# Kernel optimization log

Measured on AMD Instinct MI355X. Metric: run time of the kernel, lower is better.

## Reference

```python
import jax, jax.numpy as jnp
import numpy as np

B, H, W, C, F = 8, 128, 128, 256, 256

def setup_inputs() -> dict:
    key = jax.random.key(0)
    k1, k2, k3 = jax.random.split(key, 3)
    x = jax.random.normal(k1, (B, H, W, C), dtype=jnp.float32)
    style = jax.random.normal(k2, (B, 1, 1, C), dtype=jnp.float32)
    # he_uniform over fan_in = 3*3*C
    limit = np.sqrt(6.0 / (3 * 3 * C)).astype(np.float32)
    kernel = jax.random.uniform(k3, (3, 3, C, F), dtype=jnp.float32, minval=-limit, maxval=limit)
    return {"x": x, "style": style, "kernel": kernel}

def reference(x, style, kernel):
    b, h, w_, c = x.shape
    f = kernel.shape[-1]
    # per-sample modulation: [B,1,1,C,1] * [1,3,3,C,F] -> [B,3,3,C,F]
    wmod = kernel[None] * (style[..., None] + 1.0)
    demod = jnp.sqrt(jnp.sum(jnp.square(wmod), axis=(1, 2, 3), keepdims=True) + 1e-8)
    wmod = wmod / demod
    # grouped conv trick: x -> [1, B*C, H, W], filters -> [3,3,C,B*F], groups=B
    xg = jnp.transpose(x, (0, 3, 1, 2)).reshape(1, b * c, h, w_)
    wf = jnp.transpose(wmod, (1, 2, 3, 0, 4)).reshape(3, 3, c, b * f)
    y = jax.lax.conv_general_dilated(
        xg, wf, window_strides=(1, 1), padding='SAME',
        dimension_numbers=('NCHW', 'HWIO', 'NCHW'),
        feature_group_count=b)
    y = y.reshape(b, f, h, w_)
    return jnp.transpose(y, (0, 2, 3, 1))
```

## Files before the change

kernel.cpp:

```cpp
#include <hip/hip_runtime.h>
#include <hip/hip_bf16.h>


#define NB 8
#define NH 128
#define NW 128
#define NC 256
#define NF 256

typedef __attribute__((ext_vector_type(8))) short bf16x8;
typedef __attribute__((ext_vector_type(4))) float f32x4;

#define PA 2080
#define A_ROW (4 * PA)
#define A_BYTES (3 * A_ROW)
#define B_BUF (4 * PA)
#define LDS_BYTES (A_BYTES + 2 * B_BUF)

__device__ __forceinline__ ushort f2bf(float v) {
    union { ushort u; __hip_bfloat16 h; } o;
    o.h = __float2bfloat16(v);
    return o.u;
}

__device__ __forceinline__ void gload16(const ushort* g, const char* l) {
    __builtin_amdgcn_global_load_lds(
        (const __attribute__((address_space(1))) void*)g,
        (__attribute__((address_space(3))) void*)l,
        16, 0, 0);
}

__global__ void k_cvt(const float* __restrict__ x, ushort* __restrict__ xbf) {
    size_t i = ((size_t)blockIdx.x * 256 + threadIdx.x) * 8;
    float4 a = *(const float4*)(x + i);
    float4 b = *(const float4*)(x + i + 4);
    union { ushort s[8]; uint4 u; } o;
    o.s[0] = f2bf(a.x); o.s[1] = f2bf(a.y);
    o.s[2] = f2bf(a.z); o.s[3] = f2bf(a.w);
    o.s[4] = f2bf(b.x); o.s[5] = f2bf(b.y);
    o.s[6] = f2bf(b.z); o.s[7] = f2bf(b.w);
    *(uint4*)(xbf + i) = o.u;
}

__global__ void k_modw(const float* __restrict__ kern, const float* __restrict__ style,
                       ushort* __restrict__ wm) {
    int b = blockIdx.x >> 8;
    int f = blockIdx.x & 255;
    int c = threadIdx.x;
    float s = style[b * 256 + c] + 1.0f;
    float w[9];
    float acc = 0.f;
#pragma unroll
    for (int t = 0; t < 9; ++t) {
        w[t] = kern[(t * 256 + c) * 256 + f] * s;
        acc += w[t] * w[t];
    }
#pragma unroll
    for (int off = 32; off; off >>= 1) acc += __shfl_down(acc, off);
    __shared__ float part[4];
    if ((threadIdx.x & 63) == 0) part[threadIdx.x >> 6] = acc;
    __syncthreads();
    float total = part[0] + part[1] + part[2] + part[3];
    float inv = 1.0f / sqrtf(total + 1e-8f);
#pragma unroll
    for (int t = 0; t < 9; ++t) {
        wm[(((b * 9 + t) * 256 + f) * 256) + c] = f2bf(w[t] * inv);
    }
}

__global__ void __launch_bounds__(256)
k_conv(const ushort* __restrict__ xbf, const ushort* __restrict__ wm,
       float* __restrict__ out) {
    const int bidx = blockIdx.x;
    const int b    = bidx & 7;
    const int rest = bidx >> 3;
    const int fh   = rest & 1;
    const int h    = rest >> 1;

    __shared__ __align__(16) char smem[LDS_BYTES];
    char* As = smem;
    char* Bs = smem + A_BYTES;

    const int tid = threadIdx.x;
    const int wave = tid >> 6, lane = tid & 63;
    const int wm_ = wave & 1, wn_ = wave >> 1;
    const int lrow = lane & 15;
    const int quad = lane >> 4;

    {
        const uint4 z = {0, 0, 0, 0};
        for (int i = tid; i < A_BYTES / 16; i += 256) ((uint4*)As)[i] = z;
    }
    __syncthreads();

    f32x4 acc[4][4];
    const f32x4 zero4 = {0.f, 0.f, 0.f, 0.f};
#pragma unroll
    for (int mi = 0; mi < 4; ++mi)
#pragma unroll
        for (int ni = 0; ni < 4; ++ni) acc[mi][ni] = zero4;

    const ushort* xb_base = xbf + (size_t)b * 128 * 128 * 256;
    const ushort* wm_base = wm + ((size_t)b * 9) * 256 * 256 + (size_t)fh * 128 * 256;

    for (int c0 = 0; c0 < 256; c0 += 32) {
#pragma unroll
        for (int i = 0; i < 6; ++i) {
            int L = wave * 6 + i;
            int dh = L >> 3, rem = L & 7;
            int p = rem >> 1, half = rem & 1;
            int hp = h + dh - 1;
            if (hp >= 0 && hp < 128) {
                int w = half * 64 + lane;
                const ushort* g = xb_base + ((size_t)hp * 128 + w) * 256 + c0 + p * 8;
                const char* l = As + dh * A_ROW + p * PA + 16 + half * 1024;
                gload16(g, l);
            }
        }
        {
#pragma unroll
            for (int i = 0; i < 2; ++i) {
                int s = wave * 2 + i;
                int p = s >> 1, halfp = s & 1;
                int f = halfp * 64 + lane;
                const ushort* g = wm_base + ((size_t)(0 * 256) + f) * 256 + c0 + p * 8;
                const char* l = Bs + p * PA + halfp * 1024;
                gload16(g, l);
            }
        }
        __syncthreads();

#pragma unroll
        for (int tap = 0; tap < 9; ++tap) {
            const int dh = tap / 3, dw = tap % 3;
            const int cur = tap & 1;
            if (tap < 8) {
                int nxt = (tap + 1) & 1;
#pragma unroll
                for (int i = 0; i < 2; ++i) {
                    int s = wave * 2 + i;
                    int p = s >> 1, halfp = s & 1;
                    int f = halfp * 64 + lane;
                    const ushort* g = wm_base + ((size_t)((tap + 1) * 256) + f) * 256 + c0 + p * 8;
                    const char* l = Bs + nxt * B_BUF + p * PA + halfp * 1024;
                    gload16(g, l);
                }
            }
            bf16x8 af[4], bfr[4];
#pragma unroll
            for (int ni = 0; ni < 4; ++ni) {
                int f = wn_ * 64 + ni * 16 + lrow;
                bfr[ni] = *(const bf16x8*)(Bs + cur * B_BUF + quad * PA + f * 16);
            }
#pragma unroll
            for (int mi = 0; mi < 4; ++mi) {
                int s = wm_ * 64 + mi * 16 + lrow + dw;
                af[mi] = *(const bf16x8*)(As + dh * A_ROW + quad * PA + s * 16);
            }
#pragma unroll
            for (int mi = 0; mi < 4; ++mi)
#pragma unroll
                for (int ni = 0; ni < 4; ++ni)
                    acc[mi][ni] = __builtin_amdgcn_mfma_f32_16x16x32_bf16(
                        af[mi], bfr[ni], acc[mi][ni], 0, 0, 0);
            __syncthreads();
        }
    }

    float* obase = out + (((size_t)b * 128 + h) * 128) * 256 + fh * 128;
#pragma unroll
    for (int mi = 0; mi < 4; ++mi) {
        int wrow = wm_ * 64 + mi * 16 + quad * 4;
#pragma unroll
        for (int ni = 0; ni < 4; ++ni) {
            int f = wn_ * 64 + ni * 16 + lrow;
            f32x4 v = acc[mi][ni];
#pragma unroll
            for (int r = 0; r < 4; ++r) {
                obase[(size_t)(wrow + r) * 256 + f] = v[r];
            }
        }
    }
}

extern "C" void kernel_launch(void* const* d_in, const int* in_sizes, int n_in,
                              void* d_out, int out_size, void* d_ws, size_t ws_size,
                              hipStream_t stream) {
    const float* x     = (const float*)d_in[0];
    const float* style = (const float*)d_in[1];
    const float* kern  = (const float*)d_in[2];
    float* out = (float*)d_out;

    ushort* xbf  = (ushort*)d_ws;
    ushort* wmod = xbf + (size_t)NB * NH * NW * NC;

    k_cvt<<<(NB * NH * NW * NC) / (256 * 8), 256, 0, stream>>>(x, xbf);
    k_modw<<<NB * NF, 256, 0, stream>>>(kern, style, wmod);
    k_conv<<<NB * NH * 2, 256, 0, stream>>>(xbf, wmod, out);
}
```

Baseline: 436.9 us.

## Stream conv weights from global into registers and double-buffer input tiles

The conv kernel no longer stages modulated weights in LDS. Each lane now loads its B fragments straight from global memory into a three-deep register ring, prefetched two taps ahead, and the freed LDS double-buffers the input tile across channel chunks. This drops the per-tap __syncthreads to one barrier per 32-channel chunk, and launch bounds now ask for 3 blocks per CU. Weight modulation is split into a per-(b,f) demodulation kernel and a tiled, coalesced-write modulation kernel. The trade-offs are higher register pressure, and the new 8-block demod kernel runs serially with little parallelism.

```diff
diff --git a/kernel.cpp b/kernel.cpp
--- a/kernel.cpp
+++ b/kernel.cpp
@@ -13,11 +13,10 @@
 
 #define PA 2080
 #define A_ROW (4 * PA)
-#define A_BYTES (3 * A_ROW)
-#define B_BUF (4 * PA)
-#define LDS_BYTES (A_BYTES + 2 * B_BUF)
-
-__device__ __forceinline__ ushort f2bf(float v) {
+#define A_BUF (3 * A_ROW)
+#define LDS_BYTES (2 * A_BUF)
+
+static __device__ __forceinline__ ushort f2bf(float v) {
     union { ushort u; __hip_bfloat16 h; } o;
     o.h = __float2bfloat16(v);
     return o.u;
@@ -42,33 +41,54 @@
     *(uint4*)(xbf + i) = o.u;
 }
 
-__global__ void k_modw(const float* __restrict__ kern, const float* __restrict__ style,
-                       ushort* __restrict__ wm) {
-    int b = blockIdx.x >> 8;
-    int f = blockIdx.x & 255;
-    int c = threadIdx.x;
-    float s = style[b * 256 + c] + 1.0f;
-    float w[9];
+__global__ void k_demod(const float* __restrict__ kern, const float* __restrict__ style,
+                        float* __restrict__ invd) {
+    int b = blockIdx.x;
+    int f = threadIdx.x;
     float acc = 0.f;
 #pragma unroll
     for (int t = 0; t < 9; ++t) {
-        w[t] = kern[(t * 256 + c) * 256 + f] * s;
-        acc += w[t] * w[t];
-    }
-#pragma unroll
-    for (int off = 32; off; off >>= 1) acc += __shfl_down(acc, off);
-    __shared__ float part[4];
-    if ((threadIdx.x & 63) == 0) part[threadIdx.x >> 6] = acc;
+        const float* kp = kern + (size_t)t * 256 * 256 + f;
+#pragma unroll 8
+        for (int c = 0; c < 256; ++c) {
+            float s = style[b * 256 + c] + 1.0f;
+            float w = kp[(size_t)c * 256] * s;
+            acc += w * w;
+        }
+    }
+    invd[b * 256 + f] = 1.0f / sqrtf(acc + 1e-8f);
+}
+
+__global__ void k_wmod(const float* __restrict__ kern, const float* __restrict__ style,
+                       const float* __restrict__ invd, ushort* __restrict__ wm) {
+    int blk = blockIdx.x;
+    int fc = blk & 3;
+    int t  = (blk >> 2) % 9;
+    int b  = blk / 36;
+    int f0 = fc * 64;
+    __shared__ ushort tile[64 * 264];
+    int fl = threadIdx.x & 63;
+    int cq = threadIdx.x >> 6;
+    float dv = invd[b * 256 + f0 + fl];
+    const float* kp = kern + (size_t)t * 256 * 256 + f0 + fl;
+#pragma unroll 4
+    for (int cc = 0; cc < 64; ++cc) {
+        int c = cq * 64 + cc;
+        float s = style[b * 256 + c] + 1.0f;
+        tile[fl * 264 + c] = f2bf(kp[(size_t)c * 256] * s * dv);
+    }
     __syncthreads();
-    float total = part[0] + part[1] + part[2] + part[3];
-    float inv = 1.0f / sqrtf(total + 1e-8f);
-#pragma unroll
-    for (int t = 0; t < 9; ++t) {
-        wm[(((b * 9 + t) * 256 + f) * 256) + c] = f2bf(w[t] * inv);
-    }
-}
-
-__global__ void __launch_bounds__(256)
+    int f  = threadIdx.x >> 2;
+    int c8 = threadIdx.x & 3;
+    ushort* dst = wm + (((size_t)(b * 9 + t) * 256) + f0 + f) * 256;
+#pragma unroll
+    for (int j = 0; j < 8; ++j) {
+        int c = (c8 + j * 4) * 8;
+        *(uint4*)(dst + c) = *(const uint4*)(tile + f * 264 + c);
+    }
+}
+
+__global__ void __launch_bounds__(256, 3)
 k_conv(const ushort* __restrict__ xbf, const ushort* __restrict__ wm,
        float* __restrict__ out) {
     const int bidx = blockIdx.x;
@@ -78,8 +98,6 @@
     const int h    = rest >> 1;
 
     __shared__ __align__(16) char smem[LDS_BYTES];
-    char* As = smem;
-    char* Bs = smem + A_BYTES;
 
     const int tid = threadIdx.x;
     const int wave = tid >> 6, lane = tid & 63;
@@ -89,9 +107,20 @@
 
     {
         const uint4 z = {0, 0, 0, 0};
-        for (int i = tid; i < A_BYTES / 16; i += 256) ((uint4*)As)[i] = z;
-    }
-    __syncthreads();
+        for (int i = tid; i < LDS_BYTES / 16; i += 256) ((uint4*)smem)[i] = z;
+    }
+
+    const ushort* pB[4];
+#pragma unroll
+    for (int ni = 0; ni < 4; ++ni) {
+        int f = fh * 128 + wn_ * 64 + ni * 16 + lrow;
+        pB[ni] = wm + ((size_t)(b * 9) * 256 + f) * 256 + quad * 8;
+    }
+    bf16x8 breg[3][4];
+#pragma unroll
+    for (int ni = 0; ni < 4; ++ni) breg[0][ni] = *(const bf16x8*)(pB[ni]);
+#pragma unroll
+    for (int ni = 0; ni < 4; ++ni) breg[1][ni] = *(const bf16x8*)(pB[ni] + 65536);
 
     f32x4 acc[4][4];
     const f32x4 zero4 = {0.f, 0.f, 0.f, 0.f};
@@ -101,70 +130,68 @@
         for (int ni = 0; ni < 4; ++ni) acc[mi][ni] = zero4;
 
     const ushort* xb_base = xbf + (size_t)b * 128 * 128 * 256;
-    const ushort* wm_base = wm + ((size_t)b * 9) * 256 * 256 + (size_t)fh * 128 * 256;
-
-    for (int c0 = 0; c0 < 256; c0 += 32) {
-#pragma unroll
-        for (int i = 0; i < 6; ++i) {
-            int L = wave * 6 + i;
-            int dh = L >> 3, rem = L & 7;
-            int p = rem >> 1, half = rem & 1;
-            int hp = h + dh - 1;
-            if (hp >= 0 && hp < 128) {
-                int w = half * 64 + lane;
-                const ushort* g = xb_base + ((size_t)hp * 128 + w) * 256 + c0 + p * 8;
-                const char* l = As + dh * A_ROW + p * PA + 16 + half * 1024;
-                gload16(g, l);
-            }
-        }
-        {
-#pragma unroll
-            for (int i = 0; i < 2; ++i) {
-                int s = wave * 2 + i;
-                int p = s >> 1, halfp = s & 1;
-                int f = halfp * 64 + lane;
-                const ushort* g = wm_base + ((size_t)(0 * 256) + f) * 256 + c0 + p * 8;
-                const char* l = Bs + p * PA + halfp * 1024;
-                gload16(g, l);
-            }
-        }
+
+    __syncthreads();
+
+#pragma unroll
+    for (int i = 0; i < 6; ++i) {
+        int L = wave * 6 + i;
+        int dh = L >> 3, rem = L & 7;
+        int p = rem >> 1, half = rem & 1;
+        int hp = h + dh - 1;
+        if (hp >= 0 && hp < 128) {
+            const ushort* g = xb_base + ((size_t)hp * 128 + half * 64 + lane) * 256 + p * 8;
+            const char* l = smem + dh * A_ROW + p * PA + 16 + half * 1024;
+            gload16(g, l);
+        }
+    }
+
+    for (int k = 0; k < 8; ++k) {
         __syncthreads();
-
-#pragma unroll
-        for (int tap = 0; tap < 9; ++tap) {
-            const int dh = tap / 3, dw = tap % 3;
-            const int cur = tap & 1;
-            if (tap < 8) {
-                int nxt = (tap + 1) & 1;
-#pragma unroll
-                for (int i = 0; i < 2; ++i) {
-                    int s = wave * 2 + i;
-                    int p = s >> 1, halfp = s & 1;
-                    int f = halfp * 64 + lane;
-                    const ushort* g = wm_base + ((size_t)((tap + 1) * 256) + f) * 256 + c0 + p * 8;
-                    const char* l = Bs + nxt * B_BUF + p * PA + halfp * 1024;
+        if (k < 7) {
+            char* dstbuf = smem + ((k + 1) & 1) * A_BUF;
+            int c0 = (k + 1) * 32;
+#pragma unroll
+            for (int i = 0; i < 6; ++i) {
+                int L = wave * 6 + i;
+                int dh = L >> 3, rem = L & 7;
+                int p = rem >> 1, half = rem & 1;
+                int hp = h + dh - 1;
+                if (hp >= 0 && hp < 128) {
+                    const ushort* g = xb_base + ((size_t)hp * 128 + half * 64 + lane) * 256 + c0 + p * 8;
+                    const char* l = dstbuf + dh * A_ROW + p * PA + 16 + half * 1024;
                     gload16(g, l);
                 }
             }
-            bf16x8 af[4], bfr[4];
-#pragma unroll
-            for (int ni = 0; ni < 4; ++ni) {
-                int f = wn_ * 64 + ni * 16 + lrow;
-                bfr[ni] = *(const bf16x8*)(Bs + cur * B_BUF + quad * PA + f * 16);
-            }
+        }
+        const char* abase = smem + (k & 1) * A_BUF;
+#pragma unroll
+        for (int t = 0; t < 9; ++t) {
+            const int dh = t / 3, dw = t % 3;
+            if (t < 7) {
+#pragma unroll
+                for (int ni = 0; ni < 4; ++ni)
+                    breg[(t + 2) % 3][ni] = *(const bf16x8*)(pB[ni] + (t + 2) * 65536);
+            } else if (k < 7) {
+#pragma unroll
+                for (int ni = 0; ni < 4; ++ni)
+                    breg[(t + 2) % 3][ni] = *(const bf16x8*)(pB[ni] + (t - 7) * 65536 + 32);
+            }
+            bf16x8 af[4];
 #pragma unroll
             for (int mi = 0; mi < 4; ++mi) {
                 int s = wm_ * 64 + mi * 16 + lrow + dw;
-                af[mi] = *(const bf16x8*)(As + dh * A_ROW + quad * PA + s * 16);
+                af[mi] = *(const bf16x8*)(abase + dh * A_ROW + quad * PA + s * 16);
             }
 #pragma unroll
             for (int mi = 0; mi < 4; ++mi)
 #pragma unroll
                 for (int ni = 0; ni < 4; ++ni)
                     acc[mi][ni] = __builtin_amdgcn_mfma_f32_16x16x32_bf16(
-                        af[mi], bfr[ni], acc[mi][ni], 0, 0, 0);
-            __syncthreads();
-        }
+                        af[mi], breg[t % 3][ni], acc[mi][ni], 0, 0, 0);
+        }
+#pragma unroll
+        for (int ni = 0; ni < 4; ++ni) pB[ni] += 32;
     }
 
     float* obase = out + (((size_t)b * 128 + h) * 128) * 256 + fh * 128;
@@ -193,8 +220,10 @@
 
     ushort* xbf  = (ushort*)d_ws;
     ushort* wmod = xbf + (size_t)NB * NH * NW * NC;
+    float*  invd = (float*)(wmod + (size_t)NB * 9 * NF * NC);
 
     k_cvt<<<(NB * NH * NW * NC) / (256 * 8), 256, 0, stream>>>(x, xbf);
-    k_modw<<<NB * NF, 256, 0, stream>>>(kern, style, wmod);
+    k_demod<<<NB, 256, 0, stream>>>(kern, style, invd);
+    k_wmod<<<NB * 9 * 4, 256, 0, stream>>>(kern, style, invd, wmod);
     k_conv<<<NB * NH * 2, 256, 0, stream>>>(xbf, wmod, out);
 }
```

Result: slower. 684.8 us (+56.7%).
